# Performance work log

Hardware: AMD Instinct MI355X
Metric: run time of the kernel (lower is better)

The kernel has to match this reference:

```python
import jax, jax.numpy as jnp
import numpy as np

N_PF, N_GW, N_SW = 60000, 300000, 60000
D_IN, D, E = 32, 64, 1_000_000


def _mk_edge(key, n_src, n_dst, n_edges):
    k1, k2 = jax.random.split(key)
    return jnp.stack([
        jax.random.randint(k1, (n_edges,), 0, n_src),
        jax.random.randint(k2, (n_edges,), 0, n_dst),
    ]).astype(jnp.int32)


def _self_edge(n):
    r = jnp.arange(n, dtype=jnp.int32)
    return jnp.stack([r, r])


def setup_inputs() -> dict:
    key = jax.random.key(0)
    ks = jax.random.split(key, 20)
    s = 0.05
    return {
        "x_pf": jax.random.normal(ks[0], (N_PF, D_IN), jnp.float32),
        "x_gw": jax.random.normal(ks[1], (N_GW, D_IN), jnp.float32),
        "x_sw": jax.random.normal(ks[2], (N_SW, D_IN), jnp.float32),
        "W1l": jax.random.normal(ks[3], (10, D, D_IN), jnp.float32) * s,
        "b1l": jax.random.normal(ks[4], (10, D), jnp.float32) * s,
        "W1r": jax.random.normal(ks[5], (10, D, D_IN), jnp.float32) * s,
        "W2l": jax.random.normal(ks[6], (10, D, D), jnp.float32) * s,
        "b2l": jax.random.normal(ks[7], (10, D), jnp.float32) * s,
        "W2r": jax.random.normal(ks[8], (10, D, D), jnp.float32) * s,
        "lin_W": jax.random.normal(ks[9], (1, D), jnp.float32) * s,
        "lin_b": jax.random.normal(ks[10], (1,), jnp.float32) * s,
        "prelu_a": jnp.float32(0.25),
        "ei_pf_gw": _mk_edge(ks[11], N_PF, N_GW, E),
        "ei_gw_pf": _mk_edge(ks[12], N_GW, N_PF, E),
        "ei_pf_sw": _mk_edge(ks[13], N_PF, N_SW, E),
        "ei_sw_pf": _mk_edge(ks[14], N_SW, N_PF, E),
        "ei_sw_gw": _mk_edge(ks[15], N_SW, N_GW, E),
        "ei_gw_sw": _mk_edge(ks[16], N_GW, N_SW, E),
        "ei_gw_gw": _mk_edge(ks[17], N_GW, N_GW, E),
        "ei_gw_self": _self_edge(N_GW),
        "ei_sw_self": _self_edge(N_SW),
        "ei_pf_self": _self_edge(N_PF),
    }


def reference(x_pf, x_gw, x_sw, W1l, b1l, W1r, W2l, b2l, W2r, lin_W, lin_b,
              prelu_a, ei_pf_gw, ei_gw_pf, ei_pf_sw, ei_sw_pf, ei_sw_gw,
              ei_gw_sw, ei_gw_gw, ei_gw_self, ei_sw_self, ei_pf_self):
    n_pf, n_gw, n_sw = x_pf.shape[0], x_gw.shape[0], x_sw.shape[0]

    def sage(x_src, x_dst, ei, Wl, bl, Wr, n_dst):
        # PyG SAGEConv: lin_l(mean_j x_j) + lin_r(x_i); lin_r has no bias
        msg = x_src[ei[0]]                                        # [E, Din]
        summed = jax.ops.segment_sum(msg, ei[1], num_segments=n_dst)
        cnt = jax.ops.segment_sum(jnp.ones(ei.shape[1], x_src.dtype), ei[1],
                                  num_segments=n_dst)
        mean = summed / jnp.maximum(cnt, 1.0)[:, None]            # [Ndst, Din]
        return mean @ Wl.T + bl + x_dst @ Wr.T

    def layer(h_pf, h_gw, h_sw, Wl, bl, Wr):
        # HeteroConv with aggr='sum' over edge types per destination node type
        out_gw = (sage(h_pf, h_gw, ei_pf_gw, Wl[0], bl[0], Wr[0], n_gw)
                  + sage(h_sw, h_gw, ei_sw_gw, Wl[4], bl[4], Wr[4], n_gw)
                  + sage(h_gw, h_gw, ei_gw_gw, Wl[6], bl[6], Wr[6], n_gw)
                  + sage(h_gw, h_gw, ei_gw_self, Wl[7], bl[7], Wr[7], n_gw))
        out_pf = (sage(h_gw, h_pf, ei_gw_pf, Wl[1], bl[1], Wr[1], n_pf)
                  + sage(h_sw, h_pf, ei_sw_pf, Wl[3], bl[3], Wr[3], n_pf)
                  + sage(h_pf, h_pf, ei_pf_self, Wl[9], bl[9], Wr[9], n_pf))
        out_sw = (sage(h_pf, h_sw, ei_pf_sw, Wl[2], bl[2], Wr[2], n_sw)
                  + sage(h_gw, h_sw, ei_gw_sw, Wl[5], bl[5], Wr[5], n_sw)
                  + sage(h_sw, h_sw, ei_sw_self, Wl[8], bl[8], Wr[8], n_sw))
        return out_pf, out_gw, out_sw

    h_pf, h_gw, h_sw = layer(x_pf, x_gw, x_sw, W1l, b1l, W1r)
    h_pf, h_gw, h_sw = jax.nn.relu(h_pf), jax.nn.relu(h_gw), jax.nn.relu(h_sw)
    h_pf, h_gw, h_sw = layer(h_pf, h_gw, h_sw, W2l, b2l, W2r)
    h_pf, h_gw, h_sw = jax.nn.relu(h_pf), jax.nn.relu(h_gw), jax.nn.relu(h_sw)

    def prelu(v):
        return jnp.where(v >= 0, v, prelu_a * v)

    out_gw = prelu(h_gw @ lin_W.T + lin_b)   # [N_GW, 1]
    out_sw = prelu(h_sw @ lin_W.T + lin_b)   # [N_SW, 1]
    return out_gw, out_sw, h_pf
```

## Files before the change

kernel.cpp:

```cpp
#include <hip/hip_runtime.h>

typedef __attribute__((ext_vector_type(8))) short short8;
typedef __attribute__((ext_vector_type(4))) float floatx4;

#define N_PF 60000
#define N_GW 300000
#define N_SW 60000
#define EPT 1000000
#define TOTE 7000000
#define L_CNT 1140000
#define SPAN 4096
#define N_B 279
#define CHSZ 4096
#define NCH 1709

__device__ __forceinline__ unsigned short f2bf(float f) {
  unsigned u = __float_as_uint(f);
  u = (u + 0x7FFF + ((u >> 16) & 1)) >> 16;
  return (unsigned short)u;
}
__device__ __forceinline__ float bf2f(unsigned short u) {
  return __uint_as_float((unsigned)u << 16);
}
__device__ __forceinline__ void acc8(float* a, short8 v) {
#pragma unroll
  for (int k = 0; k < 8; ++k) a[k] += bf2f((unsigned short)v[k]);
}

__device__ __forceinline__ int cnt_base(int et) {
  switch (et) {
    case 0: return 0;
    case 1: return 300000;
    case 2: return 360000;
    case 3: return 420000;
    case 4: return 480000;
    case 5: return 780000;
    default: return 840000;
  }
}

__device__ __forceinline__ const int* pick(const int* e0, const int* e1,
                                           const int* e2, const int* e3,
                                           const int* e4, const int* e5,
                                           const int* e6, int et) {
  switch (et) {
    case 0: return e0; case 1: return e1; case 2: return e2; case 3: return e3;
    case 4: return e4; case 5: return e5; default: return e6;
  }
}

__global__ __launch_bounds__(256) void k_cast(const float4* __restrict__ x,
                                              ushort4* __restrict__ xb, int n4) {
  int i = blockIdx.x * 256 + threadIdx.x;
  if (i < n4) {
    float4 v = x[i];
    ushort4 o;
    o.x = f2bf(v.x); o.y = f2bf(v.y); o.z = f2bf(v.z); o.w = f2bf(v.w);
    xb[i] = o;
  }
}


__global__ __launch_bounds__(256) void k_h1(
    const int* e0, const int* e1, const int* e2, const int* e3,
    const int* e4, const int* e5, const int* e6, int* __restrict__ hcnt) {
  __shared__ int hist[N_B];
  int ch = blockIdx.x, t = threadIdx.x;
  for (int i = t; i < N_B; i += 256) hist[i] = 0;
  __syncthreads();
  int base = ch * CHSZ;
  int nn = TOTE - base; if (nn > CHSZ) nn = CHSZ;
#pragma unroll
  for (int u = 0; u < CHSZ / 256; ++u) {
    int o = u * 256 + t;
    if (o < nn) {
      int gid = base + o;
      int et = gid / EPT, i2 = gid - et * EPT;
      const int* ei = pick(e0, e1, e2, e3, e4, e5, e6, et);
      int idx = cnt_base(et) + ei[EPT + i2];
      atomicAdd(&hist[idx >> 12], 1);
    }
  }
  __syncthreads();
  for (int b = t; b < N_B; b += 256) hcnt[(size_t)b * NCH + ch] = hist[b];
}

__global__ __launch_bounds__(256) void k_h2a(const int* __restrict__ hcnt,
                                             int* __restrict__ btot) {
  __shared__ int sh[4];
  int b = blockIdx.x;
  const int* c = hcnt + (size_t)b * NCH;
  int s = 0;
  for (int k = threadIdx.x; k < NCH; k += 256) s += c[k];
  for (int off = 1; off < 64; off <<= 1) s += __shfl_xor(s, off, 64);
  int lane = threadIdx.x & 63, w = threadIdx.x >> 6;
  if (lane == 0) sh[w] = s;
  __syncthreads();
  if (threadIdx.x == 0) btot[b] = sh[0] + sh[1] + sh[2] + sh[3];
}

__global__ __launch_bounds__(64) void k_h2b(const int* __restrict__ btot,
                                            int* __restrict__ bbase,
                                            int* __restrict__ Sarr) {
  int lane = threadIdx.x;
  int v[5]; int s = 0;
#pragma unroll
  for (int k = 0; k < 5; ++k) {
    int i = lane * 5 + k;
    v[k] = (i < N_B) ? btot[i] : 0;
    s += v[k];
  }
  int x = s;
  for (int off = 1; off < 64; off <<= 1) {
    int tv = __shfl_up(x, off, 64);
    if (lane >= off) x += tv;
  }
  int run = x - s;
#pragma unroll
  for (int k = 0; k < 5; ++k) {
    int i = lane * 5 + k;
    if (i < N_B) bbase[i] = run;
    run += v[k];
  }
  if (lane == 63) { bbase[N_B] = x; Sarr[L_CNT] = TOTE; }
}

__global__ __launch_bounds__(256) void k_h2c(int* __restrict__ hcnt,
                                             const int* __restrict__ bbase) {
  __shared__ int sc[256];
  int b = blockIdx.x, t = threadIdx.x;
  int* c = hcnt + (size_t)b * NCH;
  int v[7]; int s = 0;
#pragma unroll
  for (int k = 0; k < 7; ++k) {
    int i = t * 7 + k;
    v[k] = (i < NCH) ? c[i] : 0;
    s += v[k];
  }
  sc[t] = s;
  __syncthreads();
  for (int off = 1; off < 256; off <<= 1) {
    int tv = (t >= off) ? sc[t - off] : 0;
    __syncthreads();
    sc[t] += tv;
    __syncthreads();
  }
  int run = bbase[b] + sc[t] - s;
#pragma unroll
  for (int k = 0; k < 7; ++k) {
    int i = t * 7 + k;
    if (i < NCH) { int vv = v[k]; c[i] = run; run += vv; }
  }
}

__global__ __launch_bounds__(256) void k_bfill(
    const int* e0, const int* e1, const int* e2, const int* e3,
    const int* e4, const int* e5, const int* e6,
    const int* __restrict__ hcnt, unsigned* __restrict__ part) {
  __shared__ int hist[N_B];
  __shared__ int segs[N_B];
  __shared__ int curb[N_B];
  __shared__ int gbase[N_B];
  __shared__ int sc[256];
  __shared__ unsigned long long stg[CHSZ];
  int ch = blockIdx.x, t = threadIdx.x;
  for (int i = t; i < N_B; i += 256) hist[i] = 0;
  __syncthreads();
  int base = ch * CHSZ;
  int nn = TOTE - base; if (nn > CHSZ) nn = CHSZ;
#pragma unroll
  for (int u = 0; u < CHSZ / 256; ++u) {
    int o = u * 256 + t;
    if (o < nn) {
      int gid = base + o;
      int et = gid / EPT, i2 = gid - et * EPT;
      const int* ei = pick(e0, e1, e2, e3, e4, e5, e6, et);
      int idx = cnt_base(et) + ei[EPT + i2];
      atomicAdd(&hist[idx >> 12], 1);
    }
  }
  __syncthreads();
  int v0 = (2 * t < N_B) ? hist[2 * t] : 0;
  int v1 = (2 * t + 1 < N_B) ? hist[2 * t + 1] : 0;
  int s = v0 + v1;
  sc[t] = s;
  __syncthreads();
  for (int off = 1; off < 256; off <<= 1) {
    int tv = (t >= off) ? sc[t - off] : 0;
    __syncthreads();
    sc[t] += tv;
    __syncthreads();
  }
  int excl = sc[t] - s;
  if (2 * t < N_B) { segs[2 * t] = excl; curb[2 * t] = excl; }
  if (2 * t + 1 < N_B) { segs[2 * t + 1] = excl + v0; curb[2 * t + 1] = excl + v0; }
  for (int b = t; b < N_B; b += 256) gbase[b] = hcnt[(size_t)b * NCH + ch];
  __syncthreads();
#pragma unroll
  for (int u = 0; u < CHSZ / 256; ++u) {
    int o = u * 256 + t;
    if (o < nn) {
      int gid = base + o;
      int et = gid / EPT, i2 = gid - et * EPT;
      const int* ei = pick(e0, e1, e2, e3, e4, e5, e6, et);
      int dst = ei[EPT + i2];
      int src = ei[i2];
      int idx = cnt_base(et) + dst;
      unsigned long long p = ((unsigned long long)idx << 32) | (unsigned)src;
      int r = atomicAdd(&curb[idx >> 12], 1);
      stg[r] = p;
    }
  }
  __syncthreads();
  for (int sdx = t; sdx < nn; sdx += 256) {
    unsigned long long p = stg[sdx];
    int idx = (int)(p >> 32);
    int b = idx >> 12;
    unsigned ent = ((unsigned)(idx & 4095) << 19) | (unsigned)(p & 0x7FFFF);
    part[(size_t)gbase[b] + (sdx - segs[b])] = ent;
  }
}

__global__ __launch_bounds__(1024) void k_cfill(
    const unsigned* __restrict__ part, const int* __restrict__ bbase,
    int* __restrict__ Sarr, int* __restrict__ col) {
  __shared__ int hist[SPAN];
  __shared__ int wt[16];
  int t = threadIdx.x;
  int lane = t & 63, wv = t >> 6;
  int b = blockIdx.x;
  int lo = b * SPAN;
  int span_n = L_CNT - lo; if (span_n > SPAN) span_n = SPAN;
  int s0 = bbase[b], s1 = bbase[b + 1];
  ((int4*)hist)[t] = (int4){0, 0, 0, 0};
  __syncthreads();
  for (int j = s0 + t; j < s1; j += 1024) {
    int local = (int)(part[j] >> 19);
    atomicAdd(&hist[local], 1);
  }
  __syncthreads();
  int4 v = ((int4*)hist)[t];
  int s = v.x + v.y + v.z + v.w;
  int x = s;
#pragma unroll
  for (int off = 1; off < 64; off <<= 1) {
    int tv = __shfl_up(x, off, 64);
    if (lane >= off) x += tv;
  }
  if (lane == 63) wt[wv] = x;
  __syncthreads();
  int woff = 0;
#pragma unroll
  for (int k = 0; k < 16; ++k) woff += (k < wv) ? wt[k] : 0;
  int run = woff + x - s;
  int4 cur4, sa4;
  cur4.x = run; sa4.x = s0 + run; run += v.x;
  cur4.y = run; sa4.y = s0 + run; run += v.y;
  cur4.z = run; sa4.z = s0 + run; run += v.z;
  cur4.w = run; sa4.w = s0 + run; run += v.w;
  __syncthreads();
  ((int4*)hist)[t] = cur4;
  if (t * 4 + 3 < span_n) {
    *(int4*)(&Sarr[lo + t * 4]) = sa4;
  } else {
    if (t * 4 + 0 < span_n) Sarr[lo + t * 4 + 0] = sa4.x;
    if (t * 4 + 1 < span_n) Sarr[lo + t * 4 + 1] = sa4.y;
    if (t * 4 + 2 < span_n) Sarr[lo + t * 4 + 2] = sa4.z;
  }
  __syncthreads();
  for (int j = s0 + t; j < s1; j += 1024) {
    unsigned p = part[j];
    int local = (int)(p >> 19);
    int r = atomicAdd(&hist[local], 1);
    col[s0 + r] = (int)(p & 0x7FFFF);
  }
}

template <int KIN, int NE>
__global__ __launch_bounds__(256) void k_prep(
    const float* __restrict__ Wl, const float* __restrict__ Wr,
    const float* __restrict__ bl, int e0, int e1, int e2, int es,
    unsigned short* __restrict__ wsw, float* __restrict__ bias) {
  constexpr int KCAT = (NE + 1) * KIN;
  int idx = blockIdx.x * 256 + threadIdx.x;
  if (idx < KCAT * 64) {
    int j = idx & 7, lane = (idx >> 3) & 63, t = idx >> 9;
    int ct = t & 3, kc = t >> 2;
    int k = kc * 32 + ((lane >> 4) << 3) + j;
    int c = ct * 16 + (lane & 15);
    int seg = k / KIN, kk = k - seg * KIN;
    float v;
    if (seg < NE) {
      int e = (seg == 0) ? e0 : (seg == 1) ? e1 : e2;
      v = Wl[((size_t)e * 64 + c) * KIN + kk];
    } else {
      v = Wl[((size_t)es * 64 + c) * KIN + kk] +
          Wr[((size_t)es * 64 + c) * KIN + kk] +
          Wr[((size_t)e0 * 64 + c) * KIN + kk] +
          Wr[((size_t)e1 * 64 + c) * KIN + kk];
      if (NE == 3) v += Wr[((size_t)e2 * 64 + c) * KIN + kk];
    }
    wsw[idx] = f2bf(v);
  } else if (idx < KCAT * 64 + 64) {
    int c = idx - KCAT * 64;
    float v = bl[e0 * 64 + c] + bl[e1 * 64 + c] + bl[es * 64 + c];
    if (NE == 3) v += bl[e2 * 64 + c];
    bias[c] = v;
  }
}

struct LType {
  const unsigned short* s0;
  const unsigned short* s1;
  const unsigned short* s2;
  int b0, b1, b2, ne;
  const unsigned short* xD;
  const unsigned short* wsw;
  const float* bias;
  void* hOut;
  int omode;
  int ntile;
};

template <int KIN>
__global__ __launch_bounds__(256) void k_layerF(
    const int* __restrict__ Sarr, const int* __restrict__ col, LType t0,
    LType t1, LType t2, const float* __restrict__ linW,
    const float* __restrict__ linb, const float* __restrict__ pa) {
  constexpr int ZSTR = 4 * KIN + 8;
  constexpr int LPR = KIN / 8;
  constexpr int G = 64 / LPR;
  __shared__ unsigned short z[4 * 16 * ZSTR];
  const int lane = threadIdx.x & 63;
  unsigned short* zw = &z[(threadIdx.x >> 6) * 16 * ZSTR];
  const int wid = (blockIdx.x * 256 + threadIdx.x) >> 6;
  const int nw = (gridDim.x * 256) >> 6;
  const int cl = lane & 15, quad = lane >> 4;
  const int g = lane / LPR;
  const int c = lane % LPR;
  const int TT = t0.ntile + t1.ntile + t2.ntile;

  for (int tile = wid; tile < TT; tile += nw) {
    LType tp;
    int lt = tile;
    if (lt < t0.ntile) tp = t0;
    else if ((lt -= t0.ntile) < t1.ntile) tp = t1;
    else { lt -= t1.ntile; tp = t2; }
    const int nb = lt * 16;
    const int ne = tp.ne;
    const int kchr = (ne + 1) * (KIN / 32);

#pragma unroll
    for (int i0 = 0; i0 < 16; i0 += G) {
      int n = nb + i0 + g;
      unsigned short* zr = &zw[(i0 + g) * ZSTR];
      *(short8*)(&zr[ne * KIN + c * 8]) =
          *(const short8*)(tp.xD + (size_t)n * KIN + c * 8);
      for (int e = 0; e < ne; ++e) {
        const unsigned short* se = (e == 0) ? tp.s0 : (e == 1) ? tp.s1 : tp.s2;
        int be = (e == 0) ? tp.b0 : (e == 1) ? tp.b1 : tp.b2;
        int s = Sarr[be + n];
        int t = Sarr[be + n + 1];
        float a0[8] = {0, 0, 0, 0, 0, 0, 0, 0};
        float a1[8] = {0, 0, 0, 0, 0, 0, 0, 0};
        int j = s;
        for (; j + 1 < t; j += 2) {
          int r0 = col[j], r1 = col[j + 1];
          short8 v0 = *(const short8*)(se + (size_t)r0 * KIN + c * 8);
          short8 v1 = *(const short8*)(se + (size_t)r1 * KIN + c * 8);
          acc8(a0, v0);
          acc8(a1, v1);
        }
        if (j < t) {
          int r0 = col[j];
          short8 v0 = *(const short8*)(se + (size_t)r0 * KIN + c * 8);
          acc8(a0, v0);
        }
        int cv = t - s;
        if (cv < 1) cv = 1;
        float inv = 1.0f / (float)cv;
        short8 o;
#pragma unroll
        for (int k = 0; k < 8; ++k)
          o[k] = (short)f2bf((a0[k] + a1[k]) * inv);
        *(short8*)(&zr[e * KIN + c * 8]) = o;
      }
    }
    floatx4 acc[4];
#pragma unroll
    for (int ct = 0; ct < 4; ++ct) {
      float bv = tp.bias[ct * 16 + cl];
      acc[ct] = (floatx4){bv, bv, bv, bv};
    }
    for (int kc = 0; kc < kchr; ++kc) {
      short8 a = *(const short8*)(&zw[cl * ZSTR + kc * 32 + quad * 8]);
#pragma unroll
      for (int ct = 0; ct < 4; ++ct) {
        short8 b =
            *(const short8*)(tp.wsw + ((size_t)(kc * 4 + ct) * 64 + lane) * 8);
        acc[ct] = __builtin_amdgcn_mfma_f32_16x16x32_bf16(a, b, acc[ct], 0, 0, 0);
      }
    }
    if (tp.omode == 2) {
      float p[4] = {0.f, 0.f, 0.f, 0.f};
#pragma unroll
      for (int ct = 0; ct < 4; ++ct) {
        float w = linW[ct * 16 + cl];
#pragma unroll
        for (int r = 0; r < 4; ++r) {
          float v = acc[ct][r];
          v = v > 0.f ? v : 0.f;
          p[r] += v * w;
        }
      }
#pragma unroll
      for (int off = 1; off < 16; off <<= 1) {
#pragma unroll
        for (int r = 0; r < 4; ++r) p[r] += __shfl_xor(p[r], off, 64);
      }
      if (cl == 0) {
        float lb = linb[0], al = pa[0];
        float* o = (float*)tp.hOut;
#pragma unroll
        for (int r = 0; r < 4; ++r) {
          int n = nb + quad * 4 + r;
          float v = p[r] + lb;
          o[n] = v >= 0.f ? v : al * v;
        }
      }
    } else if (tp.omode == 1) {
#pragma unroll
      for (int ct = 0; ct < 4; ++ct)
#pragma unroll
        for (int r = 0; r < 4; ++r) {
          int n = nb + quad * 4 + r;
          float v = acc[ct][r];
          ((float*)tp.hOut)[(size_t)n * 64 + ct * 16 + cl] = v > 0.f ? v : 0.f;
        }
    } else {
#pragma unroll
      for (int ct = 0; ct < 4; ++ct)
#pragma unroll
        for (int r = 0; r < 4; ++r) {
          int n = nb + quad * 4 + r;
          float v = acc[ct][r];
          ((unsigned short*)tp.hOut)[(size_t)n * 64 + ct * 16 + cl] =
              f2bf(v > 0.f ? v : 0.f);
        }
    }
  }
}

extern "C" void kernel_launch(void* const* d_in, const int* in_sizes, int n_in,
                              void* d_out, int out_size, void* d_ws,
                              size_t ws_size, hipStream_t stream) {
  const float* x_pf = (const float*)d_in[0];
  const float* x_gw = (const float*)d_in[1];
  const float* x_sw = (const float*)d_in[2];
  const float* W1l = (const float*)d_in[3];
  const float* b1l = (const float*)d_in[4];
  const float* W1r = (const float*)d_in[5];
  const float* W2l = (const float*)d_in[6];
  const float* b2l = (const float*)d_in[7];
  const float* W2r = (const float*)d_in[8];
  const float* linW = (const float*)d_in[9];
  const float* linb = (const float*)d_in[10];
  const float* pa = (const float*)d_in[11];
  const int* e0 = (const int*)d_in[12];
  const int* e1 = (const int*)d_in[13];
  const int* e2 = (const int*)d_in[14];
  const int* e3 = (const int*)d_in[15];
  const int* e4 = (const int*)d_in[16];
  const int* e5 = (const int*)d_in[17];
  const int* e6 = (const int*)d_in[18];
  float* out = (float*)d_out;

  char* w = (char*)d_ws;
  size_t off = 0;
  auto alloc = [&](size_t bytes) -> void* {
    void* p = w + off;
    off += bytes;
    off = (off + 255) & ~(size_t)255;
    return p;
  };
  unsigned* part = (unsigned*)alloc((size_t)TOTE * 4);
  int* col = (int*)alloc((size_t)TOTE * 4);
  int* Sarr = (int*)alloc((size_t)(L_CNT + 1) * 4);
  int* hcnt = (int*)alloc((size_t)N_B * NCH * 4);
  int* btot = (int*)alloc((N_B + 1) * 4);
  int* bbase = (int*)alloc((N_B + 1) * 4);
  unsigned short* xb_pf = (unsigned short*)alloc((size_t)N_PF * 32 * 2);
  unsigned short* xb_gw = (unsigned short*)alloc((size_t)N_GW * 32 * 2);
  unsigned short* xb_sw = (unsigned short*)alloc((size_t)N_SW * 32 * 2);
  unsigned short* h1_pf = (unsigned short*)alloc((size_t)N_PF * 64 * 2);
  unsigned short* h1_gw = (unsigned short*)alloc((size_t)N_GW * 64 * 2);
  unsigned short* h1_sw = (unsigned short*)alloc((size_t)N_SW * 64 * 2);
  unsigned short* w1gw = (unsigned short*)alloc(128 * 64 * 2);
  unsigned short* w1pf = (unsigned short*)alloc(96 * 64 * 2);
  unsigned short* w1sw = (unsigned short*)alloc(96 * 64 * 2);
  unsigned short* w2gw = (unsigned short*)alloc(256 * 64 * 2);
  unsigned short* w2pf = (unsigned short*)alloc(192 * 64 * 2);
  unsigned short* w2sw = (unsigned short*)alloc(192 * 64 * 2);
  float* bs1gw = (float*)alloc(64 * 4);
  float* bs1pf = (float*)alloc(64 * 4);
  float* bs1sw = (float*)alloc(64 * 4);
  float* bs2gw = (float*)alloc(64 * 4);
  float* bs2pf = (float*)alloc(64 * 4);
  float* bs2sw = (float*)alloc(64 * 4);

  k_cast<<<(N_PF * 8 + 255) / 256, 256, 0, stream>>>((const float4*)x_pf,
                                                     (ushort4*)xb_pf, N_PF * 8);
  k_cast<<<(N_GW * 8 + 255) / 256, 256, 0, stream>>>((const float4*)x_gw,
                                                     (ushort4*)xb_gw, N_GW * 8);
  k_cast<<<(N_SW * 8 + 255) / 256, 256, 0, stream>>>((const float4*)x_sw,
                                                     (ushort4*)xb_sw, N_SW * 8);

  k_h1<<<NCH, 256, 0, stream>>>(e0, e1, e2, e3, e4, e5, e6, hcnt);
  k_h2a<<<N_B, 256, 0, stream>>>(hcnt, btot);
  k_h2b<<<1, 64, 0, stream>>>(btot, bbase, Sarr);
  k_h2c<<<N_B, 256, 0, stream>>>(hcnt, bbase);
  k_bfill<<<NCH, 256, 0, stream>>>(e0, e1, e2, e3, e4, e5, e6, hcnt, part);
  k_cfill<<<N_B, 1024, 0, stream>>>(part, bbase, Sarr, col);

  k_prep<32, 3><<<(128 * 64 + 64 + 255) / 256, 256, 0, stream>>>(
      W1l, W1r, b1l, 0, 4, 6, 7, w1gw, bs1gw);
  k_prep<32, 2><<<(96 * 64 + 64 + 255) / 256, 256, 0, stream>>>(
      W1l, W1r, b1l, 1, 3, 0, 9, w1pf, bs1pf);
  k_prep<32, 2><<<(96 * 64 + 64 + 255) / 256, 256, 0, stream>>>(
      W1l, W1r, b1l, 2, 5, 0, 8, w1sw, bs1sw);
  k_prep<64, 3><<<(256 * 64 + 64 + 255) / 256, 256, 0, stream>>>(
      W2l, W2r, b2l, 0, 4, 6, 7, w2gw, bs2gw);
  k_prep<64, 2><<<(192 * 64 + 64 + 255) / 256, 256, 0, stream>>>(
      W2l, W2r, b2l, 1, 3, 0, 9, w2pf, bs2pf);
  k_prep<64, 2><<<(192 * 64 + 64 + 255) / 256, 256, 0, stream>>>(
      W2l, W2r, b2l, 2, 5, 0, 8, w2sw, bs2sw);

  LType a0{xb_pf, xb_sw, xb_gw, 0, 480000, 840000, 3,
           xb_gw, w1gw, bs1gw, h1_gw, 0, N_GW / 16};
  LType a1{xb_gw, xb_sw, nullptr, 300000, 420000, 0, 2,
           xb_pf, w1pf, bs1pf, h1_pf, 0, N_PF / 16};
  LType a2{xb_pf, xb_gw, nullptr, 360000, 780000, 0, 2,
           xb_sw, w1sw, bs1sw, h1_sw, 0, N_SW / 16};
  k_layerF<32><<<1024, 256, 0, stream>>>(Sarr, col, a0, a1, a2, linW, linb, pa);

  LType c0{h1_pf, h1_sw, h1_gw, 0, 480000, 840000, 3,
           h1_gw, w2gw, bs2gw, out, 2, N_GW / 16};
  LType c1{h1_gw, h1_sw, nullptr, 300000, 420000, 0, 2,
           h1_pf, w2pf, bs2pf, out + 360000, 1, N_PF / 16};
  LType c2{h1_pf, h1_gw, nullptr, 360000, 780000, 0, 2,
           h1_sw, w2sw, bs2sw, out + N_GW, 2, N_SW / 16};
  k_layerF<64><<<1024, 256, 0, stream>>>(Sarr, col, c0, c1, c2, linW, linb, pa);
}
```

Before: 697.4 us.

## Load destination features directly into MFMA registers and raise layer-kernel occupancy

Destination-node features now go straight from global memory into MFMA A-operand registers instead of passing through LDS. This shrinks each wave's LDS tile from 4*KIN to 3*KIN columns. The CSR row bounds for all edge types are loaded up front, and the edge-type loop is unrolled so the gather loads can overlap. Launch bounds gain a min-blocks hint and the grids grow (2048 and 1536 blocks) to raise occupancy for the latency-bound gather, at the risk of register pressure and spills.

```diff
diff --git a/kernel.cpp b/kernel.cpp
--- a/kernel.cpp
+++ b/kernel.cpp
@@ -322,14 +322,15 @@
   int ntile;
 };
 
-template <int KIN>
-__global__ __launch_bounds__(256) void k_layerF(
+template <int KIN, int MINW>
+__global__ __launch_bounds__(256, MINW) void k_layerF(
     const int* __restrict__ Sarr, const int* __restrict__ col, LType t0,
     LType t1, LType t2, const float* __restrict__ linW,
     const float* __restrict__ linb, const float* __restrict__ pa) {
-  constexpr int ZSTR = 4 * KIN + 8;
+  constexpr int ZSTR = 3 * KIN + 8;
   constexpr int LPR = KIN / 8;
   constexpr int G = 64 / LPR;
+  constexpr int KD = KIN / 32;
   __shared__ unsigned short z[4 * 16 * ZSTR];
   const int lane = threadIdx.x & 63;
   unsigned short* zw = &z[(threadIdx.x >> 6) * 16 * ZSTR];
@@ -348,42 +349,53 @@
     else { lt -= t1.ntile; tp = t2; }
     const int nb = lt * 16;
     const int ne = tp.ne;
-    const int kchr = (ne + 1) * (KIN / 32);
+    const int klds = ne * KD;
+
+    short8 adst[KD];
+#pragma unroll
+    for (int kd = 0; kd < KD; ++kd)
+      adst[kd] = *(const short8*)(tp.xD + (size_t)(nb + cl) * KIN +
+                                  kd * 32 + quad * 8);
 
 #pragma unroll
     for (int i0 = 0; i0 < 16; i0 += G) {
       int n = nb + i0 + g;
       unsigned short* zr = &zw[(i0 + g) * ZSTR];
-      *(short8*)(&zr[ne * KIN + c * 8]) =
-          *(const short8*)(tp.xD + (size_t)n * KIN + c * 8);
-      for (int e = 0; e < ne; ++e) {
-        const unsigned short* se = (e == 0) ? tp.s0 : (e == 1) ? tp.s1 : tp.s2;
-        int be = (e == 0) ? tp.b0 : (e == 1) ? tp.b1 : tp.b2;
-        int s = Sarr[be + n];
-        int t = Sarr[be + n + 1];
-        float a0[8] = {0, 0, 0, 0, 0, 0, 0, 0};
-        float a1[8] = {0, 0, 0, 0, 0, 0, 0, 0};
-        int j = s;
-        for (; j + 1 < t; j += 2) {
-          int r0 = col[j], r1 = col[j + 1];
-          short8 v0 = *(const short8*)(se + (size_t)r0 * KIN + c * 8);
-          short8 v1 = *(const short8*)(se + (size_t)r1 * KIN + c * 8);
-          acc8(a0, v0);
-          acc8(a1, v1);
+      int s0v = Sarr[tp.b0 + n], t0v = Sarr[tp.b0 + n + 1];
+      int s1v = Sarr[tp.b1 + n], t1v = Sarr[tp.b1 + n + 1];
+      int s2v = 0, t2v = 0;
+      if (ne == 3) { s2v = Sarr[tp.b2 + n]; t2v = Sarr[tp.b2 + n + 1]; }
+#pragma unroll
+      for (int E = 0; E < 3; ++E) {
+        if (E < ne) {
+          const unsigned short* se =
+              (E == 0) ? tp.s0 : (E == 1) ? tp.s1 : tp.s2;
+          int s = (E == 0) ? s0v : (E == 1) ? s1v : s2v;
+          int t = (E == 0) ? t0v : (E == 1) ? t1v : t2v;
+          float a0[8] = {0, 0, 0, 0, 0, 0, 0, 0};
+          float a1[8] = {0, 0, 0, 0, 0, 0, 0, 0};
+          int j = s;
+          for (; j + 1 < t; j += 2) {
+            int r0 = col[j], r1 = col[j + 1];
+            short8 v0 = *(const short8*)(se + (size_t)r0 * KIN + c * 8);
+            short8 v1 = *(const short8*)(se + (size_t)r1 * KIN + c * 8);
+            acc8(a0, v0);
+            acc8(a1, v1);
+          }
+          if (j < t) {
+            int r0 = col[j];
+            short8 v0 = *(const short8*)(se + (size_t)r0 * KIN + c * 8);
+            acc8(a0, v0);
+          }
+          int cv = t - s;
+          if (cv < 1) cv = 1;
+          float inv = 1.0f / (float)cv;
+          short8 o;
+#pragma unroll
+          for (int k = 0; k < 8; ++k)
+            o[k] = (short)f2bf((a0[k] + a1[k]) * inv);
+          *(short8*)(&zr[E * KIN + c * 8]) = o;
         }
-        if (j < t) {
-          int r0 = col[j];
-          short8 v0 = *(const short8*)(se + (size_t)r0 * KIN + c * 8);
-          acc8(a0, v0);
-        }
-        int cv = t - s;
-        if (cv < 1) cv = 1;
-        float inv = 1.0f / (float)cv;
-        short8 o;
-#pragma unroll
-        for (int k = 0; k < 8; ++k)
-          o[k] = (short)f2bf((a0[k] + a1[k]) * inv);
-        *(short8*)(&zr[e * KIN + c * 8]) = o;
       }
     }
     floatx4 acc[4];
@@ -392,8 +404,19 @@
       float bv = tp.bias[ct * 16 + cl];
       acc[ct] = (floatx4){bv, bv, bv, bv};
     }
-    for (int kc = 0; kc < kchr; ++kc) {
+    for (int kc = 0; kc < klds; ++kc) {
       short8 a = *(const short8*)(&zw[cl * ZSTR + kc * 32 + quad * 8]);
+#pragma unroll
+      for (int ct = 0; ct < 4; ++ct) {
+        short8 b =
+            *(const short8*)(tp.wsw + ((size_t)(kc * 4 + ct) * 64 + lane) * 8);
+        acc[ct] = __builtin_amdgcn_mfma_f32_16x16x32_bf16(a, b, acc[ct], 0, 0, 0);
+      }
+    }
+#pragma unroll
+    for (int kd = 0; kd < KD; ++kd) {
+      short8 a = adst[kd];
+      int kc = klds + kd;
 #pragma unroll
       for (int ct = 0; ct < 4; ++ct) {
         short8 b =
@@ -541,7 +564,8 @@
            xb_pf, w1pf, bs1pf, h1_pf, 0, N_PF / 16};
   LType a2{xb_pf, xb_gw, nullptr, 360000, 780000, 0, 2,
            xb_sw, w1sw, bs1sw, h1_sw, 0, N_SW / 16};
-  k_layerF<32><<<1024, 256, 0, stream>>>(Sarr, col, a0, a1, a2, linW, linb, pa);
+  k_layerF<32, 8><<<2048, 256, 0, stream>>>(Sarr, col, a0, a1, a2, linW, linb,
+                                            pa);
 
   LType c0{h1_pf, h1_sw, h1_gw, 0, 480000, 840000, 3,
            h1_gw, w2gw, bs2gw, out, 2, N_GW / 16};
@@ -549,5 +573,6 @@
            h1_pf, w2pf, bs2pf, out + 360000, 1, N_PF / 16};
   LType c2{h1_pf, h1_gw, nullptr, 360000, 780000, 0, 2,
            h1_sw, w2sw, bs2sw, out + N_GW, 2, N_SW / 16};
-  k_layerF<64><<<1024, 256, 0, stream>>>(Sarr, col, c0, c1, c2, linW, linb, pa);
-}
+  k_layerF<64, 6><<<1536, 256, 0, stream>>>(Sarr, col, c0, c1, c2, linW, linb,
+                                            pa);
+}
```

Measured after the change: 677.3 us. 1.03x faster.
